# Performance work log

Hardware: AMD Instinct MI355X
Metric: run time of the kernel (lower is better)

## Reference

```python
import jax, jax.numpy as jnp
import numpy as np

N = 100000      # nodes
E = 1600000     # edges (avg degree 16)
F_IN = 128
HID = 128
LAT = 64


def gat_conv(x, src, dst, W, a_src, a_dst, b, n):
    """PyG GATConv (single aggregation): lin -> per-edge LeakyReLU(0.2) attention
    -> segment softmax over incoming edges of each dst node -> weighted scatter-add -> bias.
    W: [F_in, H*C], a_src/a_dst: [H, C], b: [H*C] (concat) or [C] (H=1 either way)."""
    H, C = a_src.shape
    h = (x @ W).reshape(n, H, C)                              # [N,H,C]
    al_s = jnp.einsum('nhc,hc->nh', h, a_src)                 # [N,H]
    al_d = jnp.einsum('nhc,hc->nh', h, a_dst)                 # [N,H]
    e = jax.nn.leaky_relu(al_s[src] + al_d[dst], 0.2)         # [E,H]
    emax = jax.lax.stop_gradient(jax.ops.segment_max(e, dst, num_segments=n))
    ee = jnp.exp(e - emax[dst])                               # stable segment softmax
    den = jax.ops.segment_sum(ee, dst, num_segments=n)
    alpha = ee / (den[dst] + 1e-16)                           # [E,H]
    out = jax.ops.segment_sum(h[src] * alpha[:, :, None], dst, num_segments=n)  # [N,H,C]
    return out.reshape(n, H * C) + b


def setup_inputs() -> dict:
    key = jax.random.key(0)
    ks = jax.random.split(key, 24)
    s = 0.05
    inp = {
        'x': jax.random.normal(ks[0], (N, F_IN), jnp.float32),
        'edge_index': jax.random.randint(ks[1], (2, E), 0, N, jnp.int64),
        # layer 0 GATConv (in -> hid, H=1) + self linear
        'W0': jax.random.normal(ks[2], (F_IN, HID), jnp.float32) * s,
        'a_src0': jax.random.normal(ks[3], (1, HID), jnp.float32) * s,
        'a_dst0': jax.random.normal(ks[4], (1, HID), jnp.float32) * s,
        'b0': jnp.zeros((HID,), jnp.float32),
        'slW0': jax.random.normal(ks[5], (F_IN, HID), jnp.float32) * s,
        'slb0': jnp.zeros((HID,), jnp.float32),
        # layer 1 GATConv (hid -> hid, H=1) + self linear
        'W1': jax.random.normal(ks[6], (HID, HID), jnp.float32) * s,
        'a_src1': jax.random.normal(ks[7], (1, HID), jnp.float32) * s,
        'a_dst1': jax.random.normal(ks[8], (1, HID), jnp.float32) * s,
        'b1': jnp.zeros((HID,), jnp.float32),
        'slW1': jax.random.normal(ks[9], (HID, HID), jnp.float32) * s,
        'slb1': jnp.zeros((HID,), jnp.float32),
        # mu / logvar heads (hid -> lat, H=1, concat=False)
        'Wmu': jax.random.normal(ks[10], (HID, LAT), jnp.float32) * s,
        'a_src_mu': jax.random.normal(ks[11], (1, LAT), jnp.float32) * s,
        'a_dst_mu': jax.random.normal(ks[12], (1, LAT), jnp.float32) * s,
        'b_mu': jnp.zeros((LAT,), jnp.float32),
        'Wlv': jax.random.normal(ks[13], (HID, LAT), jnp.float32) * s,
        'a_src_lv': jax.random.normal(ks[14], (1, LAT), jnp.float32) * s,
        'a_dst_lv': jax.random.normal(ks[15], (1, LAT), jnp.float32) * s,
        'b_lv': jnp.zeros((LAT,), jnp.float32),
    }
    return inp


def reference(x, edge_index, W0, a_src0, a_dst0, b0, slW0, slb0,
              W1, a_src1, a_dst1, b1, slW1, slb1,
              Wmu, a_src_mu, a_dst_mu, b_mu, Wlv, a_src_lv, a_dst_lv, b_lv):
    src, dst = edge_index[0], edge_index[1]
    loop = jnp.arange(N, dtype=edge_index.dtype)
    src_sl = jnp.concatenate([src, loop])   # layers with add_self_loops=True
    dst_sl = jnp.concatenate([dst, loop])
    # layer 0: GATConv(add_self_loops=False) + Linear, then LeakyReLU(0.01)
    h = gat_conv(x, src, dst, W0, a_src0, a_dst0, b0, N) + x @ slW0 + slb0
    h = jax.nn.leaky_relu(h, 0.01)
    # layer 1: GATConv(default self loops) + Linear, then LeakyReLU(0.01)
    h = gat_conv(h, src_sl, dst_sl, W1, a_src1, a_dst1, b1, N) + h @ slW1 + slb1
    h = jax.nn.leaky_relu(h, 0.01)
    mu = gat_conv(h, src_sl, dst_sl, Wmu, a_src_mu, a_dst_mu, b_mu, N)
    logvar = gat_conv(h, src_sl, dst_sl, Wlv, a_src_lv, a_dst_lv, b_lv, N)
    return (mu, logvar)
```

## Files before the change

### kernel.cpp

```cpp
#include <hip/hip_runtime.h>
#include <cstdint>
#include <cstddef>

__device__ __forceinline__ float bf2f(unsigned short u) {
  return __uint_as_float(((unsigned)u) << 16);
}
__device__ __forceinline__ unsigned short f2bf(float f) {
  unsigned u = __float_as_uint(f);
  u = (u + 0x7FFFu + ((u >> 16) & 1u)) >> 16;
  return (unsigned short)u;
}

typedef __attribute__((ext_vector_type(8))) short bf16x8;
typedef __attribute__((ext_vector_type(4))) float f32x4;

__global__ void detect_kernel(const int* __restrict__ ei, int* __restrict__ flag) {
  int any = 0;
  for (int j = threadIdx.x; j < 4096; j += 256) any |= (ei[2 * j + 1] != 0);
  if (any) atomicOr(flag, 1);
}

__device__ __forceinline__ int edge_src(const int* ei, int f, int e, int i) {
  return f ? ei[i] : ei[2 * (size_t)i];
}
__device__ __forceinline__ int edge_dst(const int* ei, int f, int e, int i) {
  return f ? ei[(size_t)e + i] : ei[2 * (size_t)e + 2 * (size_t)i];
}

__global__ void hist_kernel(const int* __restrict__ ei, const int* __restrict__ flag,
                            int* __restrict__ cnt, int e) {
  int i = blockIdx.x * blockDim.x + threadIdx.x;
  if (i < e) atomicAdd(&cnt[edge_dst(ei, *flag, e, i)], 1);
}

__global__ void scan_block(const int* __restrict__ cnt, int* __restrict__ rp,
                           int* __restrict__ bsum, int n) {
  __shared__ int lds[256];
  const int t = threadIdx.x;
  const int base = blockIdx.x * 1024 + t * 4;
  int v0 = (base     < n) ? cnt[base]     : 0;
  int v1 = (base + 1 < n) ? cnt[base + 1] : 0;
  int v2 = (base + 2 < n) ? cnt[base + 2] : 0;
  int v3 = (base + 3 < n) ? cnt[base + 3] : 0;
  int s = v0 + v1 + v2 + v3;
  lds[t] = s;
  __syncthreads();
  for (int off = 1; off < 256; off <<= 1) {
    int y = (t >= off) ? lds[t - off] : 0;
    __syncthreads();
    lds[t] += y;
    __syncthreads();
  }
  int excl = lds[t] - s;
  if (base     < n) rp[base]     = excl;
  if (base + 1 < n) rp[base + 1] = excl + v0;
  if (base + 2 < n) rp[base + 2] = excl + v0 + v1;
  if (base + 3 < n) rp[base + 3] = excl + v0 + v1 + v2;
  if (t == 255) bsum[blockIdx.x] = lds[255];
}

__global__ void scan_tops(int* __restrict__ bsum, int* __restrict__ rp, int nb, int n) {
  __shared__ int lds[128];
  const int t = threadIdx.x;
  int v = (t < nb) ? bsum[t] : 0;
  lds[t] = v;
  __syncthreads();
  for (int off = 1; off < 128; off <<= 1) {
    int y = (t >= off) ? lds[t - off] : 0;
    __syncthreads();
    lds[t] += y;
    __syncthreads();
  }
  if (t < nb) bsum[t] = lds[t] - v;
  if (t == 127) rp[n] = lds[127];
}

__global__ void scan_add(int* __restrict__ rp, const int* __restrict__ bsum, int n) {
  const int base = blockIdx.x * 1024 + threadIdx.x * 4;
  const int add = bsum[blockIdx.x];
#pragma unroll
  for (int i = 0; i < 4; ++i)
    if (base + i < n) rp[base + i] += add;
}

#define NB 128

__global__ void bucket_hist(const int* __restrict__ ei, const int* __restrict__ flag,
                            int* __restrict__ bhist, int e, int W) {
  __shared__ int lh[NB];
  const int t = threadIdx.x;
  if (t < NB) lh[t] = 0;
  __syncthreads();
  const int base = blockIdx.x * 4096;
  const int f = *flag;
  for (int j = t; j < 4096; j += 256) {
    int i = base + j;
    if (i < e) atomicAdd(&lh[edge_dst(ei, f, e, i) / W], 1);
  }
  __syncthreads();
  if (t < NB && lh[t]) atomicAdd(&bhist[t], lh[t]);
}

__global__ void bucket_scan(const int* __restrict__ bhist, int* __restrict__ boffs,
                            int* __restrict__ bcur) {
  __shared__ int lds[NB];
  const int t = threadIdx.x;
  int v = bhist[t];
  lds[t] = v;
  __syncthreads();
  for (int off = 1; off < NB; off <<= 1) {
    int y = (t >= off) ? lds[t - off] : 0;
    __syncthreads();
    lds[t] += y;
    __syncthreads();
  }
  int excl = lds[t] - v;
  boffs[t] = excl;
  bcur[t] = excl;
  if (t == NB - 1) boffs[NB] = lds[NB - 1];
}

__global__ void bucket_scatter(const int* __restrict__ ei, const int* __restrict__ flag,
                               int* __restrict__ bcur, int2* __restrict__ ebuf,
                               int e, int W) {
  __shared__ int lh[NB];
  __shared__ int lbase[NB];
  const int t = threadIdx.x;
  if (t < NB) lh[t] = 0;
  __syncthreads();
  const int base = blockIdx.x * 4096;
  const int f = *flag;
  for (int j = t; j < 4096; j += 256) {
    int i = base + j;
    if (i < e) atomicAdd(&lh[edge_dst(ei, f, e, i) / W], 1);
  }
  __syncthreads();
  if (t < NB) {
    lbase[t] = lh[t] ? atomicAdd(&bcur[t], lh[t]) : 0;
    lh[t] = 0;
  }
  __syncthreads();
  for (int j = t; j < 4096; j += 256) {
    int i = base + j;
    if (i < e) {
      int d = edge_dst(ei, f, e, i);
      int s = edge_src(ei, f, e, i);
      int b = d / W;
      int off = atomicAdd(&lh[b], 1);
      ebuf[lbase[b] + off] = make_int2(s, d);
    }
  }
}

__global__ void bucket_fill(const int2* __restrict__ ebuf, const int* __restrict__ boffs,
                            const int* __restrict__ rp, int* __restrict__ col,
                            int n, int W) {
  __shared__ int cur[1024];
  const int b = blockIdx.x;
  const int lo = b * W;
  const int nn = min(W, n - lo);
  if (nn <= 0) return;
  for (int i = threadIdx.x; i < nn; i += 256) cur[i] = rp[lo + i];
  __syncthreads();
  const int beg = boffs[b], end = boffs[b + 1];
  for (int p = beg + threadIdx.x; p < end; p += 256) {
    int2 sd = ebuf[p];
    int pos = atomicAdd(&cur[sd.y - lo], 1);
    col[pos] = sd.x;
  }
}

__global__ void pack_mfma_b(const float* __restrict__ Wf, unsigned short* __restrict__ Wpk) {
  int i = blockIdx.x * 256 + threadIdx.x;
  if (i >= 2048) return;
  int lane = i & 63, nt = (i >> 6) & 7, ks = i >> 9;
  int nn = lane & 15, q = lane >> 4;
  int k0 = ks * 32 + q * 8, col = nt * 16 + nn;
  unsigned short o[8];
#pragma unroll
  for (int j = 0; j < 8; ++j) o[j] = f2bf(Wf[(size_t)(k0 + j) * 128 + col]);
  uint4 u;
  u.x = (unsigned)o[0] | ((unsigned)o[1] << 16);
  u.y = (unsigned)o[2] | ((unsigned)o[3] << 16);
  u.z = (unsigned)o[4] | ((unsigned)o[5] << 16);
  u.w = (unsigned)o[6] | ((unsigned)o[7] << 16);
  *(uint4*)(Wpk + (size_t)i * 8) = u;
}

__global__ void pack_mfma_head(const float* __restrict__ Wmu, const float* __restrict__ Wlv,
                               unsigned short* __restrict__ Wpk) {
  int i = blockIdx.x * 256 + threadIdx.x;
  if (i >= 2048) return;
  int lane = i & 63, nt = (i >> 6) & 7, ks = i >> 9;
  int nn = lane & 15, q = lane >> 4;
  int k0 = ks * 32 + q * 8, col = nt * 16 + nn;
  unsigned short o[8];
#pragma unroll
  for (int j = 0; j < 8; ++j) {
    float v = (col < 64) ? Wmu[(size_t)(k0 + j) * 64 + col]
                         : Wlv[(size_t)(k0 + j) * 64 + (col - 64)];
    o[j] = f2bf(v);
  }
  uint4 u;
  u.x = (unsigned)o[0] | ((unsigned)o[1] << 16);
  u.y = (unsigned)o[2] | ((unsigned)o[3] << 16);
  u.z = (unsigned)o[4] | ((unsigned)o[5] << 16);
  u.w = (unsigned)o[6] | ((unsigned)o[7] << 16);
  *(uint4*)(Wpk + (size_t)i * 8) = u;
}

template <bool HEAD>
__launch_bounds__(256)
__global__ void gemm_mfma(const float* __restrict__ X, const unsigned short* __restrict__ Wpk,
                          const float* __restrict__ a0s, const float* __restrict__ a0d,
                          const float* __restrict__ a1s, const float* __restrict__ a1d,
                          unsigned short* __restrict__ hg,
                          float* __restrict__ als, float* __restrict__ ald, int n) {
  const int wave = threadIdx.x >> 6;
  const int lane = threadIdx.x & 63;
  const int nidx = lane & 15, q = lane >> 4;
  const int r0 = blockIdx.x * 64 + wave * 16;
  const int arow = r0 + nidx;

  f32x4 acc[8];
#pragma unroll
  for (int nt = 0; nt < 8; ++nt) acc[nt] = (f32x4){0.f, 0.f, 0.f, 0.f};

#pragma unroll
  for (int ks = 0; ks < 4; ++ks) {
    union { unsigned short u[8]; bf16x8 v; } af;
    if (arow < n) {
      const float* xp = X + (size_t)arow * 128 + ks * 32 + q * 8;
      float4 a = *(const float4*)xp;
      float4 b = *(const float4*)(xp + 4);
      af.u[0] = f2bf(a.x); af.u[1] = f2bf(a.y); af.u[2] = f2bf(a.z); af.u[3] = f2bf(a.w);
      af.u[4] = f2bf(b.x); af.u[5] = f2bf(b.y); af.u[6] = f2bf(b.z); af.u[7] = f2bf(b.w);
    } else {
#pragma unroll
      for (int j = 0; j < 8; ++j) af.u[j] = 0;
    }
    const unsigned short* bp = Wpk + ((size_t)ks * 8 * 64 + lane) * 8;
#pragma unroll
    for (int nt = 0; nt < 8; ++nt) {
      bf16x8 bfm = *(const bf16x8*)(bp + (size_t)nt * 64 * 8);
      acc[nt] = __builtin_amdgcn_mfma_f32_16x16x32_bf16(af.v, bfm, acc[nt], 0, 0, 0);
    }
  }

  float dv[8][4];
#pragma unroll
  for (int nt = 0; nt < 8; ++nt) {
#pragma unroll
    for (int r = 0; r < 4; ++r) {
      unsigned short rb = f2bf(acc[nt][r]);
      dv[nt][r] = bf2f(rb);
      int row = r0 + q * 4 + r;
      if (row < n) hg[(size_t)row * 128 + nt * 16 + nidx] = rb;
    }
  }

  if constexpr (!HEAD) {
    float ps[4] = {0, 0, 0, 0}, pd[4] = {0, 0, 0, 0};
#pragma unroll
    for (int nt = 0; nt < 8; ++nt) {
      float as_ = a0s[nt * 16 + nidx];
      float ad_ = a0d[nt * 16 + nidx];
#pragma unroll
      for (int r = 0; r < 4; ++r) {
        ps[r] = fmaf(dv[nt][r], as_, ps[r]);
        pd[r] = fmaf(dv[nt][r], ad_, pd[r]);
      }
    }
#pragma unroll
    for (int r = 0; r < 4; ++r) {
#pragma unroll
      for (int o = 8; o > 0; o >>= 1) {
        ps[r] += __shfl_xor(ps[r], o, 64);
        pd[r] += __shfl_xor(pd[r], o, 64);
      }
      int row = r0 + q * 4 + r;
      if (nidx == 0 && row < n) { als[row] = ps[r]; ald[row] = pd[r]; }
    }
  } else {
    float pms[4] = {0, 0, 0, 0}, pmd[4] = {0, 0, 0, 0};
    float pls[4] = {0, 0, 0, 0}, pld[4] = {0, 0, 0, 0};
#pragma unroll
    for (int nt = 0; nt < 4; ++nt) {
      float as_ = a0s[nt * 16 + nidx];
      float ad_ = a0d[nt * 16 + nidx];
#pragma unroll
      for (int r = 0; r < 4; ++r) {
        pms[r] = fmaf(dv[nt][r], as_, pms[r]);
        pmd[r] = fmaf(dv[nt][r], ad_, pmd[r]);
      }
    }
#pragma unroll
    for (int nt = 4; nt < 8; ++nt) {
      float as_ = a1s[(nt - 4) * 16 + nidx];
      float ad_ = a1d[(nt - 4) * 16 + nidx];
#pragma unroll
      for (int r = 0; r < 4; ++r) {
        pls[r] = fmaf(dv[nt][r], as_, pls[r]);
        pld[r] = fmaf(dv[nt][r], ad_, pld[r]);
      }
    }
#pragma unroll
    for (int r = 0; r < 4; ++r) {
#pragma unroll
      for (int o = 8; o > 0; o >>= 1) {
        pms[r] += __shfl_xor(pms[r], o, 64);
        pmd[r] += __shfl_xor(pmd[r], o, 64);
        pls[r] += __shfl_xor(pls[r], o, 64);
        pld[r] += __shfl_xor(pld[r], o, 64);
      }
      int row = r0 + q * 4 + r;
      if (nidx == 0 && row < n) {
        ((float2*)als)[row] = make_float2(pms[r], pls[r]);
        ((float2*)ald)[row] = make_float2(pmd[r], pld[r]);
      }
    }
  }
}

template <int C, bool YBF>
__launch_bounds__(256)
__global__ void gemm_k128(const float* Xv, const float* __restrict__ Wf,
                          const float* __restrict__ biasf, void* Yv, int n) {
  constexpr int TC = C / 32;
  __shared__ float xs[64 * 32];
  __shared__ float wsm[32 * C];
  const int t = threadIdx.x;
  const int tc = t & 31;
  const int trg = t >> 5;
  const int row0 = blockIdx.x * 64;

  float acc[8][TC];
#pragma unroll
  for (int i = 0; i < 8; ++i)
#pragma unroll
    for (int c = 0; c < TC; ++c) acc[i][c] = 0.f;

  for (int kc = 0; kc < 128; kc += 32) {
    {
      const int r = t >> 2;
      const int j = (t & 3) * 8;
      const int row = row0 + r;
      float v[8];
      if (row < n) {
        const float* xp = Xv + (size_t)row * 128 + kc + j;
        float4 a = *(const float4*)xp;
        float4 b = *(const float4*)(xp + 4);
        v[0] = a.x; v[1] = a.y; v[2] = a.z; v[3] = a.w;
        v[4] = b.x; v[5] = b.y; v[6] = b.z; v[7] = b.w;
      } else {
#pragma unroll
        for (int q = 0; q < 8; ++q) v[q] = 0.f;
      }
      *(float4*)&xs[r * 32 + j]     = make_float4(v[0], v[1], v[2], v[3]);
      *(float4*)&xs[r * 32 + j + 4] = make_float4(v[4], v[5], v[6], v[7]);
    }
    {
      constexpr int per = (32 * C) / 256;
      const float* wp = Wf + (size_t)kc * C + t * per;
      float* wl = wsm + t * per;
#pragma unroll
      for (int q = 0; q < per; q += 4) *(float4*)(wl + q) = *(const float4*)(wp + q);
    }
    __syncthreads();
#pragma unroll
    for (int k = 0; k < 32; k += 4) {
      float wv[4][TC];
#pragma unroll
      for (int k2 = 0; k2 < 4; ++k2) {
        if constexpr (TC == 4) {
          float4 w4 = *(const float4*)&wsm[(k + k2) * C + tc * 4];
          wv[k2][0] = w4.x; wv[k2][1] = w4.y; wv[k2][2] = w4.z; wv[k2][3] = w4.w;
        } else {
          float2 w2 = *(const float2*)&wsm[(k + k2) * C + tc * 2];
          wv[k2][0] = w2.x; wv[k2][1] = w2.y;
        }
      }
#pragma unroll
      for (int i = 0; i < 8; ++i) {
        float4 x4 = *(const float4*)&xs[(trg * 8 + i) * 32 + k];
        float xa[4] = {x4.x, x4.y, x4.z, x4.w};
#pragma unroll
        for (int k2 = 0; k2 < 4; ++k2)
#pragma unroll
          for (int c = 0; c < TC; ++c)
            acc[i][c] = fmaf(xa[k2], wv[k2][c], acc[i][c]);
      }
    }
    __syncthreads();
  }
  float bv[TC];
#pragma unroll
  for (int c = 0; c < TC; ++c) bv[c] = biasf ? biasf[tc * TC + c] : 0.f;
#pragma unroll
  for (int i = 0; i < 8; ++i) {
    const int row = row0 + trg * 8 + i;
    if (row < n) {
      float r[TC];
#pragma unroll
      for (int c = 0; c < TC; ++c) r[c] = acc[i][c] + bv[c];
      if constexpr (YBF) {
        unsigned short* yp = (unsigned short*)Yv + (size_t)row * C + tc * TC;
        if constexpr (TC == 4) {
          uint2 u;
          u.x = (unsigned)f2bf(r[0]) | ((unsigned)f2bf(r[1]) << 16);
          u.y = (unsigned)f2bf(r[2]) | ((unsigned)f2bf(r[3]) << 16);
          *(uint2*)yp = u;
        } else {
          *(unsigned*)yp = (unsigned)f2bf(r[0]) | ((unsigned)f2bf(r[1]) << 16);
        }
      } else {
        float* yp = (float*)Yv + (size_t)row * C + tc * TC;
        if constexpr (TC == 4) *(float4*)yp = make_float4(r[0], r[1], r[2], r[3]);
        else                   *(float2*)yp = make_float2(r[0], r[1]);
      }
    }
  }
}

__launch_bounds__(256)
__global__ void gat_agg3(const unsigned short* __restrict__ hg,
                         const float* __restrict__ als, const float* __restrict__ aldv,
                         const int* __restrict__ rp, const int* __restrict__ col,
                         const float* __restrict__ biasf, float* __restrict__ outv,
                         const float* base, int n, int self_loop, int act) {
  const int node = blockIdx.x * 16 + (threadIdx.x >> 4);
  if (node >= n) return;
  const int g = threadIdx.x & 15;
  const int beg = rp[node];
  const int deg = rp[node + 1] - beg;
  const int total = deg + self_loop;
  const float ad = aldv[node];

  float den = 0.f;
  float acc[8];
#pragma unroll
  for (int k = 0; k < 8; ++k) acc[k] = 0.f;

  const unsigned short* hgl = hg + g * 8;

  for (int cb = 0; cb < total; cb += 16) {
    const int idx = cb + g;
    const bool valid = idx < total;
    int s = node;
    if (valid && idx < deg) s = col[beg + idx];
    float e = 0.f;
    if (valid) {
      float v = als[s] + ad;
      float l = (v > 0.f) ? v : 0.2f * v;
      e = __expf(l);
    }

    const int cnt = (total - cb < 16) ? (total - cb) : 16;
    int j = 0;
    for (; j + 4 <= cnt; j += 4) {
      float w[4]; int ss[4]; uint4 rr[4];
#pragma unroll
      for (int u = 0; u < 4; ++u) { w[u] = __shfl(e, j + u, 16); ss[u] = __shfl(s, j + u, 16); }
#pragma unroll
      for (int u = 0; u < 4; ++u) rr[u] = *(const uint4*)(hgl + (size_t)ss[u] * 128);
#pragma unroll
      for (int u = 0; u < 4; ++u) {
        den += w[u];
        acc[0] = fmaf(w[u], __uint_as_float(rr[u].x << 16),        acc[0]);
        acc[1] = fmaf(w[u], __uint_as_float(rr[u].x & 0xFFFF0000u), acc[1]);
        acc[2] = fmaf(w[u], __uint_as_float(rr[u].y << 16),        acc[2]);
        acc[3] = fmaf(w[u], __uint_as_float(rr[u].y & 0xFFFF0000u), acc[3]);
        acc[4] = fmaf(w[u], __uint_as_float(rr[u].z << 16),        acc[4]);
        acc[5] = fmaf(w[u], __uint_as_float(rr[u].z & 0xFFFF0000u), acc[5]);
        acc[6] = fmaf(w[u], __uint_as_float(rr[u].w << 16),        acc[6]);
        acc[7] = fmaf(w[u], __uint_as_float(rr[u].w & 0xFFFF0000u), acc[7]);
      }
    }
    for (; j < cnt; ++j) {
      float wj = __shfl(e, j, 16);
      int sj = __shfl(s, j, 16);
      uint4 raw = *(const uint4*)(hgl + (size_t)sj * 128);
      den += wj;
      acc[0] = fmaf(wj, __uint_as_float(raw.x << 16),        acc[0]);
      acc[1] = fmaf(wj, __uint_as_float(raw.x & 0xFFFF0000u), acc[1]);
      acc[2] = fmaf(wj, __uint_as_float(raw.y << 16),        acc[2]);
      acc[3] = fmaf(wj, __uint_as_float(raw.y & 0xFFFF0000u), acc[3]);
      acc[4] = fmaf(wj, __uint_as_float(raw.z << 16),        acc[4]);
      acc[5] = fmaf(wj, __uint_as_float(raw.z & 0xFFFF0000u), acc[5]);
      acc[6] = fmaf(wj, __uint_as_float(raw.w << 16),        acc[6]);
      acc[7] = fmaf(wj, __uint_as_float(raw.w & 0xFFFF0000u), acc[7]);
    }
  }

  const float inv = 1.f / (den + 1e-16f);
  const size_t o = (size_t)node * 128 + g * 8;
  float4 bv0 = *(const float4*)(biasf + g * 8);
  float4 bv1 = *(const float4*)(biasf + g * 8 + 4);
  float r[8];
  r[0] = acc[0] * inv + bv0.x; r[1] = acc[1] * inv + bv0.y;
  r[2] = acc[2] * inv + bv0.z; r[3] = acc[3] * inv + bv0.w;
  r[4] = acc[4] * inv + bv1.x; r[5] = acc[5] * inv + bv1.y;
  r[6] = acc[6] * inv + bv1.z; r[7] = acc[7] * inv + bv1.w;
  if (base) {
    float4 s0 = *(const float4*)(base + o);
    float4 s1 = *(const float4*)(base + o + 4);
    r[0] += s0.x; r[1] += s0.y; r[2] += s0.z; r[3] += s0.w;
    r[4] += s1.x; r[5] += s1.y; r[6] += s1.z; r[7] += s1.w;
  }
  if (act) {
#pragma unroll
    for (int k = 0; k < 8; ++k) r[k] = (r[k] > 0.f) ? r[k] : 0.01f * r[k];
  }
  *(float4*)(outv + o)     = make_float4(r[0], r[1], r[2], r[3]);
  *(float4*)(outv + o + 4) = make_float4(r[4], r[5], r[6], r[7]);
}

__launch_bounds__(256)
__global__ void gat_agg_dual(const unsigned short* __restrict__ hg,
                             const float2* __restrict__ alsH, const float2* __restrict__ aldH,
                             const int* __restrict__ rp, const int* __restrict__ col,
                             const float* __restrict__ bmu, const float* __restrict__ blv,
                             float* __restrict__ outF, int n) {
  const int node = blockIdx.x * 16 + (threadIdx.x >> 4);
  if (node >= n) return;
  const int g = threadIdx.x & 15;
  const bool isMu = g < 8;
  const int beg = rp[node];
  const int deg = rp[node + 1] - beg;
  const int total = deg + 1;
  const float2 ad = aldH[node];

  float den = 0.f;
  float acc[8];
#pragma unroll
  for (int k = 0; k < 8; ++k) acc[k] = 0.f;

  const unsigned short* hgl = hg + g * 8;

  for (int cb = 0; cb < total; cb += 16) {
    const int idx = cb + g;
    const bool valid = idx < total;
    int s = node;
    if (valid && idx < deg) s = col[beg + idx];
    float eM = 0.f, eL = 0.f;
    if (valid) {
      float2 as_ = alsH[s];
      float vm = as_.x + ad.x;
      float vl = as_.y + ad.y;
      eM = __expf((vm > 0.f) ? vm : 0.2f * vm);
      eL = __expf((vl > 0.f) ? vl : 0.2f * vl);
    }

    const int cnt = (total - cb < 16) ? (total - cb) : 16;
    int j = 0;
    for (; j + 4 <= cnt; j += 4) {
      float w[4]; int ss[4]; uint4 rr[4];
#pragma unroll
      for (int u = 0; u < 4; ++u) {
        float wm = __shfl(eM, j + u, 16), wl = __shfl(eL, j + u, 16);
        w[u] = isMu ? wm : wl;
        ss[u] = __shfl(s, j + u, 16);
      }
#pragma unroll
      for (int u = 0; u < 4; ++u) rr[u] = *(const uint4*)(hgl + (size_t)ss[u] * 128);
#pragma unroll
      for (int u = 0; u < 4; ++u) {
        den += w[u];
        acc[0] = fmaf(w[u], __uint_as_float(rr[u].x << 16),        acc[0]);
        acc[1] = fmaf(w[u], __uint_as_float(rr[u].x & 0xFFFF0000u), acc[1]);
        acc[2] = fmaf(w[u], __uint_as_float(rr[u].y << 16),        acc[2]);
        acc[3] = fmaf(w[u], __uint_as_float(rr[u].y & 0xFFFF0000u), acc[3]);
        acc[4] = fmaf(w[u], __uint_as_float(rr[u].z << 16),        acc[4]);
        acc[5] = fmaf(w[u], __uint_as_float(rr[u].z & 0xFFFF0000u), acc[5]);
        acc[6] = fmaf(w[u], __uint_as_float(rr[u].w << 16),        acc[6]);
        acc[7] = fmaf(w[u], __uint_as_float(rr[u].w & 0xFFFF0000u), acc[7]);
      }
    }
    for (; j < cnt; ++j) {
      float wm = __shfl(eM, j, 16), wl = __shfl(eL, j, 16);
      float wj = isMu ? wm : wl;
      int sj = __shfl(s, j, 16);
      uint4 raw = *(const uint4*)(hgl + (size_t)sj * 128);
      den += wj;
      acc[0] = fmaf(wj, __uint_as_float(raw.x << 16),        acc[0]);
      acc[1] = fmaf(wj, __uint_as_float(raw.x & 0xFFFF0000u), acc[1]);
      acc[2] = fmaf(wj, __uint_as_float(raw.y << 16),        acc[2]);
      acc[3] = fmaf(wj, __uint_as_float(raw.y & 0xFFFF0000u), acc[3]);
      acc[4] = fmaf(wj, __uint_as_float(raw.z << 16),        acc[4]);
      acc[5] = fmaf(wj, __uint_as_float(raw.z & 0xFFFF0000u), acc[5]);
      acc[6] = fmaf(wj, __uint_as_float(raw.w << 16),        acc[6]);
      acc[7] = fmaf(wj, __uint_as_float(raw.w & 0xFFFF0000u), acc[7]);
    }
  }

  const float inv = 1.f / (den + 1e-16f);
  const int c = (g & 7) * 8;
  const float* bb = isMu ? bmu : blv;
  float4 bv0 = *(const float4*)(bb + c);
  float4 bv1 = *(const float4*)(bb + c + 4);
  float* op = outF + (isMu ? (size_t)0 : (size_t)n * 64) + (size_t)node * 64 + c;
  *(float4*)op = make_float4(acc[0] * inv + bv0.x, acc[1] * inv + bv0.y,
                             acc[2] * inv + bv0.z, acc[3] * inv + bv0.w);
  *(float4*)(op + 4) = make_float4(acc[4] * inv + bv1.x, acc[5] * inv + bv1.y,
                                   acc[6] * inv + bv1.z, acc[7] * inv + bv1.w);
}

extern "C" void kernel_launch(void* const* d_in, const int* in_sizes, int n_in,
                              void* d_out, int out_size, void* d_ws, size_t ws_size,
                              hipStream_t stream) {
  const int N = in_sizes[0] / 128;
  const int E = in_sizes[1] / 2;
  const int W = (N + NB - 1) / NB;

  const float* x    = (const float*)d_in[0];
  const int*   ei   = (const int*)d_in[1];
  const float* W0   = (const float*)d_in[2];
  const float* as0  = (const float*)d_in[3];
  const float* ad0  = (const float*)d_in[4];
  const float* b0   = (const float*)d_in[5];
  const float* slW0 = (const float*)d_in[6];
  const float* slb0 = (const float*)d_in[7];
  const float* W1   = (const float*)d_in[8];
  const float* as1  = (const float*)d_in[9];
  const float* ad1  = (const float*)d_in[10];
  const float* b1   = (const float*)d_in[11];
  const float* slW1 = (const float*)d_in[12];
  const float* slb1 = (const float*)d_in[13];
  const float* Wmu  = (const float*)d_in[14];
  const float* asmu = (const float*)d_in[15];
  const float* admu = (const float*)d_in[16];
  const float* bmu  = (const float*)d_in[17];
  const float* Wlv  = (const float*)d_in[18];
  const float* aslv = (const float*)d_in[19];
  const float* adlv = (const float*)d_in[20];
  const float* blv  = (const float*)d_in[21];

  float*          outF = (float*)d_out;
  unsigned short* hgB  = (unsigned short*)d_out;

  char* w = (char*)d_ws;
  auto carve = [&](size_t bytes) -> char* {
    char* p = w;
    w += (bytes + 255) & ~(size_t)255;
    return p;
  };
  float*          h0    = (float*)carve((size_t)N * 128 * 4);
  unsigned short* hgHd  = (unsigned short*)carve((size_t)N * 128 * 2);
  float*          als   = (float*)carve((size_t)N * 4);
  float*          ald   = (float*)carve((size_t)N * 4);
  float2*         alsH  = (float2*)carve((size_t)N * 8);
  float2*         aldH  = (float2*)carve((size_t)N * 8);
  int*            cnt   = (int*)carve((size_t)N * 4);
  int*            rp    = (int*)carve((size_t)(N + 1) * 4);
  int*            col   = (int*)carve((size_t)E * 4);
  int*            bsum  = (int*)carve(512);
  int*            bhist = (int*)carve(NB * 4);
  int*            boffs = (int*)carve((NB + 1) * 4);
  int*            bcur  = (int*)carve(NB * 4);
  int*            flag  = (int*)carve(4);
  unsigned short* Wpk0  = (unsigned short*)carve(2048 * 8 * 2);
  unsigned short* Wpk1  = (unsigned short*)carve(2048 * 8 * 2);
  unsigned short* Wpkh  = (unsigned short*)carve(2048 * 8 * 2);
  int2*           ebuf  = (int2*)h0;

  const int gE  = (E + 255) / 256;
  const int gB4 = (E + 4095) / 4096;
  const int gG  = (N + 63) / 64;
  const int gW  = (N + 15) / 16;
  const int nb  = (N + 1023) / 1024;

  hipMemsetAsync(flag, 0, 4, stream);
  hipMemsetAsync(cnt, 0, (size_t)N * 4, stream);
  hipMemsetAsync(bhist, 0, NB * 4, stream);
  detect_kernel<<<1, 256, 0, stream>>>(ei, flag);
  hist_kernel<<<gE, 256, 0, stream>>>(ei, flag, cnt, E);
  bucket_hist<<<gB4, 256, 0, stream>>>(ei, flag, bhist, E, W);
  scan_block<<<nb, 256, 0, stream>>>(cnt, rp, bsum, N);
  scan_tops<<<1, 128, 0, stream>>>(bsum, rp, nb, N);
  scan_add<<<nb, 256, 0, stream>>>(rp, bsum, N);
  bucket_scan<<<1, NB, 0, stream>>>(bhist, boffs, bcur);
  bucket_scatter<<<gB4, 256, 0, stream>>>(ei, flag, bcur, ebuf, E, W);
  bucket_fill<<<NB, 256, 0, stream>>>(ebuf, boffs, rp, col, N, W);

  pack_mfma_b<<<8, 256, 0, stream>>>(W0, Wpk0);
  pack_mfma_b<<<8, 256, 0, stream>>>(W1, Wpk1);
  pack_mfma_head<<<8, 256, 0, stream>>>(Wmu, Wlv, Wpkh);

  gemm_mfma<false><<<gG, 256, 0, stream>>>(x, Wpk0, as0, ad0, nullptr, nullptr,
                                           hgB, als, ald, N);
  gemm_k128<128, false><<<gG, 256, 0, stream>>>(x, slW0, slb0, h0, N);
  gat_agg3<<<gW, 256, 0, stream>>>(hgB, als, ald, rp, col, b0, h0, h0, N, 0, 1);

  gemm_mfma<false><<<gG, 256, 0, stream>>>(h0, Wpk1, as1, ad1, nullptr, nullptr,
                                           hgB, als, ald, N);
  gemm_k128<128, false><<<gG, 256, 0, stream>>>(h0, slW1, slb1, h0, N);
  gat_agg3<<<gW, 256, 0, stream>>>(hgB, als, ald, rp, col, b1, h0, h0, N, 1, 1);

  gemm_mfma<true><<<gG, 256, 0, stream>>>(h0, Wpkh, asmu, admu, aslv, adlv,
                                          hgHd, (float*)alsH, (float*)aldH, N);
  gat_agg_dual<<<gW, 256, 0, stream>>>(hgHd, alsH, aldH, rp, col, bmu, blv, outF, N);
}
```

Before: 671.3 us.

## Precompute per-edge attention weights in separate kernels and prefetch next edge chunk

Adds edge_w and edge_w_dual kernels that compute exp(leaky_relu(als[src]+ald[dst])) for each CSR edge into a buffer that aliases existing workspace. The aggregation kernels then read these weights coalesced instead of doing a dependent gather of als[col] followed by exp. They also software-prefetch the next 16-edge chunk's column indices and weights while the current chunk is processed, to hide the latency of the dependent load chain. The cost is extra kernel launches plus an extra write and read of an E-sized weight array per layer, and the one-thread-per-node edge_w loop is itself uncoalesced and load-imbalanced.

After: 720.4 us. +7.3%, slower.

```diff
diff --git a/kernel.cpp b/kernel.cpp
--- a/kernel.cpp
+++ b/kernel.cpp
@@ -167,6 +167,34 @@
     int2 sd = ebuf[p];
     int pos = atomicAdd(&cur[sd.y - lo], 1);
     col[pos] = sd.x;
+  }
+}
+
+__global__ void edge_w(const float* __restrict__ als, const float* __restrict__ ald,
+                       const int* __restrict__ rp, const int* __restrict__ col,
+                       float* __restrict__ ew, int n) {
+  int i = blockIdx.x * 256 + threadIdx.x;
+  if (i >= n) return;
+  const int b = rp[i], e = rp[i + 1];
+  const float ad = ald[i];
+  for (int p = b; p < e; ++p) {
+    float v = als[col[p]] + ad;
+    ew[p] = __expf((v > 0.f) ? v : 0.2f * v);
+  }
+}
+
+__global__ void edge_w_dual(const float2* __restrict__ alsH, const float2* __restrict__ aldH,
+                            const int* __restrict__ rp, const int* __restrict__ col,
+                            float2* __restrict__ ewH, int n) {
+  int i = blockIdx.x * 256 + threadIdx.x;
+  if (i >= n) return;
+  const int b = rp[i], e = rp[i + 1];
+  const float2 ad = aldH[i];
+  for (int p = b; p < e; ++p) {
+    float2 a = alsH[col[p]];
+    float vm = a.x + ad.x, vl = a.y + ad.y;
+    ewH[p] = make_float2(__expf((vm > 0.f) ? vm : 0.2f * vm),
+                         __expf((vl > 0.f) ? vl : 0.2f * vl));
   }
 }
 
@@ -424,6 +452,7 @@
 
 __launch_bounds__(256)
 __global__ void gat_agg3(const unsigned short* __restrict__ hg,
+                         const float* __restrict__ ew,
                          const float* __restrict__ als, const float* __restrict__ aldv,
                          const int* __restrict__ rp, const int* __restrict__ col,
                          const float* __restrict__ biasf, float* __restrict__ outv,
@@ -434,7 +463,12 @@
   const int beg = rp[node];
   const int deg = rp[node + 1] - beg;
   const int total = deg + self_loop;
-  const float ad = aldv[node];
+
+  float wself = 0.f;
+  if (self_loop) {
+    float v = als[node] + aldv[node];
+    wself = __expf((v > 0.f) ? v : 0.2f * v);
+  }
 
   float den = 0.f;
   float acc[8];
@@ -443,16 +477,19 @@
 
   const unsigned short* hgl = hg + g * 8;
 
+  int sA = node; float wA = 0.f;
+  {
+    const int idx = g;
+    if (idx < deg)        { sA = col[beg + idx]; wA = ew[beg + idx]; }
+    else if (idx < total) { wA = wself; }
+  }
+
   for (int cb = 0; cb < total; cb += 16) {
-    const int idx = cb + g;
-    const bool valid = idx < total;
-    int s = node;
-    if (valid && idx < deg) s = col[beg + idx];
-    float e = 0.f;
-    if (valid) {
-      float v = als[s] + ad;
-      float l = (v > 0.f) ? v : 0.2f * v;
-      e = __expf(l);
+    int sB = node; float wB = 0.f;
+    {
+      const int idx = cb + 16 + g;
+      if (idx < deg)        { sB = col[beg + idx]; wB = ew[beg + idx]; }
+      else if (idx < total) { wB = wself; }
     }
 
     const int cnt = (total - cb < 16) ? (total - cb) : 16;
@@ -460,7 +497,7 @@
     for (; j + 4 <= cnt; j += 4) {
       float w[4]; int ss[4]; uint4 rr[4];
 #pragma unroll
-      for (int u = 0; u < 4; ++u) { w[u] = __shfl(e, j + u, 16); ss[u] = __shfl(s, j + u, 16); }
+      for (int u = 0; u < 4; ++u) { w[u] = __shfl(wA, j + u, 16); ss[u] = __shfl(sA, j + u, 16); }
 #pragma unroll
       for (int u = 0; u < 4; ++u) rr[u] = *(const uint4*)(hgl + (size_t)ss[u] * 128);
 #pragma unroll
@@ -477,8 +514,8 @@
       }
     }
     for (; j < cnt; ++j) {
-      float wj = __shfl(e, j, 16);
-      int sj = __shfl(s, j, 16);
+      float wj = __shfl(wA, j, 16);
+      int sj = __shfl(sA, j, 16);
       uint4 raw = *(const uint4*)(hgl + (size_t)sj * 128);
       den += wj;
       acc[0] = fmaf(wj, __uint_as_float(raw.x << 16),        acc[0]);
@@ -490,6 +527,7 @@
       acc[6] = fmaf(wj, __uint_as_float(raw.w << 16),        acc[6]);
       acc[7] = fmaf(wj, __uint_as_float(raw.w & 0xFFFF0000u), acc[7]);
     }
+    sA = sB; wA = wB;
   }
 
   const float inv = 1.f / (den + 1e-16f);
@@ -517,6 +555,7 @@
 
 __launch_bounds__(256)
 __global__ void gat_agg_dual(const unsigned short* __restrict__ hg,
+                             const float2* __restrict__ ewH,
                              const float2* __restrict__ alsH, const float2* __restrict__ aldH,
                              const int* __restrict__ rp, const int* __restrict__ col,
                              const float* __restrict__ bmu, const float* __restrict__ blv,
@@ -528,7 +567,14 @@
   const int beg = rp[node];
   const int deg = rp[node + 1] - beg;
   const int total = deg + 1;
-  const float2 ad = aldH[node];
+
+  float wselfM, wselfL;
+  {
+    float2 a_ = alsH[node], d_ = aldH[node];
+    float vm = a_.x + d_.x, vl = a_.y + d_.y;
+    wselfM = __expf((vm > 0.f) ? vm : 0.2f * vm);
+    wselfL = __expf((vl > 0.f) ? vl : 0.2f * vl);
+  }
 
   float den = 0.f;
   float acc[8];
@@ -537,18 +583,19 @@
 
   const unsigned short* hgl = hg + g * 8;
 
+  int sA = node; float eMA = 0.f, eLA = 0.f;
+  {
+    const int idx = g;
+    if (idx < deg)        { sA = col[beg + idx]; float2 e2 = ewH[beg + idx]; eMA = e2.x; eLA = e2.y; }
+    else if (idx < total) { eMA = wselfM; eLA = wselfL; }
+  }
+
   for (int cb = 0; cb < total; cb += 16) {
-    const int idx = cb + g;
-    const bool valid = idx < total;
-    int s = node;
-    if (valid && idx < deg) s = col[beg + idx];
-    float eM = 0.f, eL = 0.f;
-    if (valid) {
-      float2 as_ = alsH[s];
-      float vm = as_.x + ad.x;
-      float vl = as_.y + ad.y;
-      eM = __expf((vm > 0.f) ? vm : 0.2f * vm);
-      eL = __expf((vl > 0.f) ? vl : 0.2f * vl);
+    int sB = node; float eMB = 0.f, eLB = 0.f;
+    {
+      const int idx = cb + 16 + g;
+      if (idx < deg)        { sB = col[beg + idx]; float2 e2 = ewH[beg + idx]; eMB = e2.x; eLB = e2.y; }
+      else if (idx < total) { eMB = wselfM; eLB = wselfL; }
     }
 
     const int cnt = (total - cb < 16) ? (total - cb) : 16;
@@ -557,9 +604,9 @@
       float w[4]; int ss[4]; uint4 rr[4];
 #pragma unroll
       for (int u = 0; u < 4; ++u) {
-        float wm = __shfl(eM, j + u, 16), wl = __shfl(eL, j + u, 16);
+        float wm = __shfl(eMA, j + u, 16), wl = __shfl(eLA, j + u, 16);
         w[u] = isMu ? wm : wl;
-        ss[u] = __shfl(s, j + u, 16);
+        ss[u] = __shfl(sA, j + u, 16);
       }
 #pragma unroll
       for (int u = 0; u < 4; ++u) rr[u] = *(const uint4*)(hgl + (size_t)ss[u] * 128);
@@ -577,9 +624,9 @@
       }
     }
     for (; j < cnt; ++j) {
-      float wm = __shfl(eM, j, 16), wl = __shfl(eL, j, 16);
+      float wm = __shfl(eMA, j, 16), wl = __shfl(eLA, j, 16);
       float wj = isMu ? wm : wl;
-      int sj = __shfl(s, j, 16);
+      int sj = __shfl(sA, j, 16);
       uint4 raw = *(const uint4*)(hgl + (size_t)sj * 128);
       den += wj;
       acc[0] = fmaf(wj, __uint_as_float(raw.x << 16),        acc[0]);
@@ -591,6 +638,7 @@
       acc[6] = fmaf(wj, __uint_as_float(raw.w << 16),        acc[6]);
       acc[7] = fmaf(wj, __uint_as_float(raw.w & 0xFFFF0000u), acc[7]);
     }
+    sA = sB; eMA = eMB; eLA = eLB;
   }
 
   const float inv = 1.f / (den + 1e-16f);
@@ -662,11 +710,14 @@
   unsigned short* Wpk1  = (unsigned short*)carve(2048 * 8 * 2);
   unsigned short* Wpkh  = (unsigned short*)carve(2048 * 8 * 2);
   int2*           ebuf  = (int2*)h0;
+  float*          ew    = (float*)hgHd;
+  float2*         ewH   = (float2*)h0;
 
   const int gE  = (E + 255) / 256;
   const int gB4 = (E + 4095) / 4096;
   const int gG  = (N + 63) / 64;
   const int gW  = (N + 15) / 16;
+  const int gN  = (N + 255) / 256;
   const int nb  = (N + 1023) / 1024;
 
   hipMemsetAsync(flag, 0, 4, stream);
@@ -688,15 +739,18 @@
 
   gemm_mfma<false><<<gG, 256, 0, stream>>>(x, Wpk0, as0, ad0, nullptr, nullptr,
                                            hgB, als, ald, N);
+  edge_w<<<gN, 256, 0, stream>>>(als, ald, rp, col, ew, N);
   gemm_k128<128, false><<<gG, 256, 0, stream>>>(x, slW0, slb0, h0, N);
-  gat_agg3<<<gW, 256, 0, stream>>>(hgB, als, ald, rp, col, b0, h0, h0, N, 0, 1);
+  gat_agg3<<<gW, 256, 0, stream>>>(hgB, ew, als, ald, rp, col, b0, h0, h0, N, 0, 1);
 
   gemm_mfma<false><<<gG, 256, 0, stream>>>(h0, Wpk1, as1, ad1, nullptr, nullptr,
                                            hgB, als, ald, N);
+  edge_w<<<gN, 256, 0, stream>>>(als, ald, rp, col, ew, N);
   gemm_k128<128, false><<<gG, 256, 0, stream>>>(h0, slW1, slb1, h0, N);
-  gat_agg3<<<gW, 256, 0, stream>>>(hgB, als, ald, rp, col, b1, h0, h0, N, 1, 1);
+  gat_agg3<<<gW, 256, 0, stream>>>(hgB, ew, als, ald, rp, col, b1, h0, h0, N, 1, 1);
 
   gemm_mfma<true><<<gG, 256, 0, stream>>>(h0, Wpkh, asmu, admu, aslv, adlv,
                                           hgHd, (float*)alsH, (float*)aldH, N);
-  gat_agg_dual<<<gW, 256, 0, stream>>>(hgHd, alsH, aldH, rp, col, bmu, blv, outF, N);
-}
+  edge_w_dual<<<gN, 256, 0, stream>>>(alsH, aldH, rp, col, ewH, N);
+  gat_agg_dual<<<gW, 256, 0, stream>>>(hgHd, ewH, alsH, aldH, rp, col, bmu, blv, outF, N);
+}
```

## Fuse self-linear GEMM into MFMA GEMM using split-bf16 hi/lo products

Applied to the files above, without the earlier changes.

Replaces the separate fp32 SIMT self-linear GEMM with extra MFMA accumulators inside the attention-projection GEMM kernel. The input row is read once and split into bf16 hi/lo parts, and the self weights are pre-packed as hi/lo pairs. Three MFMAs (hh, lh, hl) approximate fp32 accuracy. This removes one kernel launch and a second pass over X. In exchange it adds register pressure (16 accumulators) and roughly four times the MFMA work per tile.

Result: faster. 648.8 us (-3.4%).

```diff
diff --git a/kernel.cpp b/kernel.cpp
--- a/kernel.cpp
+++ b/kernel.cpp
@@ -187,6 +187,35 @@
   *(uint4*)(Wpk + (size_t)i * 8) = u;
 }
 
+__global__ void pack_mfma_b_hilo(const float* __restrict__ Wf,
+                                 unsigned short* __restrict__ Hi,
+                                 unsigned short* __restrict__ Lo) {
+  int i = blockIdx.x * 256 + threadIdx.x;
+  if (i >= 2048) return;
+  int lane = i & 63, nt = (i >> 6) & 7, ks = i >> 9;
+  int nn = lane & 15, q = lane >> 4;
+  int k0 = ks * 32 + q * 8, col = nt * 16 + nn;
+  unsigned short oh[8], ol[8];
+#pragma unroll
+  for (int j = 0; j < 8; ++j) {
+    float v = Wf[(size_t)(k0 + j) * 128 + col];
+    unsigned short h = f2bf(v);
+    oh[j] = h;
+    ol[j] = f2bf(v - bf2f(h));
+  }
+  uint4 uh, ul;
+  uh.x = (unsigned)oh[0] | ((unsigned)oh[1] << 16);
+  uh.y = (unsigned)oh[2] | ((unsigned)oh[3] << 16);
+  uh.z = (unsigned)oh[4] | ((unsigned)oh[5] << 16);
+  uh.w = (unsigned)oh[6] | ((unsigned)oh[7] << 16);
+  ul.x = (unsigned)ol[0] | ((unsigned)ol[1] << 16);
+  ul.y = (unsigned)ol[2] | ((unsigned)ol[3] << 16);
+  ul.z = (unsigned)ol[4] | ((unsigned)ol[5] << 16);
+  ul.w = (unsigned)ol[6] | ((unsigned)ol[7] << 16);
+  *(uint4*)(Hi + (size_t)i * 8) = uh;
+  *(uint4*)(Lo + (size_t)i * 8) = ul;
+}
+
 __global__ void pack_mfma_head(const float* __restrict__ Wmu, const float* __restrict__ Wlv,
                                unsigned short* __restrict__ Wpk) {
   int i = blockIdx.x * 256 + threadIdx.x;
@@ -209,13 +238,111 @@
   *(uint4*)(Wpk + (size_t)i * 8) = u;
 }
 
-template <bool HEAD>
 __launch_bounds__(256)
-__global__ void gemm_mfma(const float* __restrict__ X, const unsigned short* __restrict__ Wpk,
-                          const float* __restrict__ a0s, const float* __restrict__ a0d,
-                          const float* __restrict__ a1s, const float* __restrict__ a1d,
-                          unsigned short* __restrict__ hg,
-                          float* __restrict__ als, float* __restrict__ ald, int n) {
+__global__ void gemm_fused(const float* __restrict__ X, const unsigned short* __restrict__ Wpk,
+                           const unsigned short* __restrict__ Sph, const unsigned short* __restrict__ Spl,
+                           const float* __restrict__ a0s, const float* __restrict__ a0d,
+                           const float* __restrict__ slb,
+                           unsigned short* __restrict__ hg, float* __restrict__ hself,
+                           float* __restrict__ als, float* __restrict__ ald, int n) {
+  const int wave = threadIdx.x >> 6;
+  const int lane = threadIdx.x & 63;
+  const int nidx = lane & 15, q = lane >> 4;
+  const int r0 = blockIdx.x * 64 + wave * 16;
+  const int arow = r0 + nidx;
+
+  f32x4 acc[8], accS[8];
+#pragma unroll
+  for (int nt = 0; nt < 8; ++nt) {
+    acc[nt]  = (f32x4){0.f, 0.f, 0.f, 0.f};
+    accS[nt] = (f32x4){0.f, 0.f, 0.f, 0.f};
+  }
+
+#pragma unroll
+  for (int ks = 0; ks < 4; ++ks) {
+    union { unsigned short u[8]; bf16x8 v; } afh, afl;
+    if (arow < n) {
+      const float* xp = X + (size_t)arow * 128 + ks * 32 + q * 8;
+      float4 a = *(const float4*)xp;
+      float4 b = *(const float4*)(xp + 4);
+      float xv[8] = {a.x, a.y, a.z, a.w, b.x, b.y, b.z, b.w};
+#pragma unroll
+      for (int j = 0; j < 8; ++j) {
+        unsigned short h = f2bf(xv[j]);
+        afh.u[j] = h;
+        afl.u[j] = f2bf(xv[j] - bf2f(h));
+      }
+    } else {
+#pragma unroll
+      for (int j = 0; j < 8; ++j) { afh.u[j] = 0; afl.u[j] = 0; }
+    }
+    const size_t base = ((size_t)ks * 8 * 64 + lane) * 8;
+    const unsigned short* bp = Wpk + base;
+    const unsigned short* ph = Sph + base;
+    const unsigned short* pl = Spl + base;
+#pragma unroll
+    for (int nt = 0; nt < 8; ++nt) {
+      bf16x8 bW = *(const bf16x8*)(bp + (size_t)nt * 64 * 8);
+      acc[nt] = __builtin_amdgcn_mfma_f32_16x16x32_bf16(afh.v, bW, acc[nt], 0, 0, 0);
+      bf16x8 bH = *(const bf16x8*)(ph + (size_t)nt * 64 * 8);
+      bf16x8 bL = *(const bf16x8*)(pl + (size_t)nt * 64 * 8);
+      accS[nt] = __builtin_amdgcn_mfma_f32_16x16x32_bf16(afh.v, bH, accS[nt], 0, 0, 0);
+      accS[nt] = __builtin_amdgcn_mfma_f32_16x16x32_bf16(afl.v, bH, accS[nt], 0, 0, 0);
+      accS[nt] = __builtin_amdgcn_mfma_f32_16x16x32_bf16(afh.v, bL, accS[nt], 0, 0, 0);
+    }
+  }
+
+  float dv[8][4];
+#pragma unroll
+  for (int nt = 0; nt < 8; ++nt) {
+#pragma unroll
+    for (int r = 0; r < 4; ++r) {
+      unsigned short rb = f2bf(acc[nt][r]);
+      dv[nt][r] = bf2f(rb);
+      int row = r0 + q * 4 + r;
+      if (row < n) hg[(size_t)row * 128 + nt * 16 + nidx] = rb;
+    }
+  }
+
+#pragma unroll
+  for (int nt = 0; nt < 8; ++nt) {
+    const float sb = slb[nt * 16 + nidx];
+#pragma unroll
+    for (int r = 0; r < 4; ++r) {
+      int row = r0 + q * 4 + r;
+      if (row < n) hself[(size_t)row * 128 + nt * 16 + nidx] = accS[nt][r] + sb;
+    }
+  }
+
+  float ps[4] = {0, 0, 0, 0}, pd[4] = {0, 0, 0, 0};
+#pragma unroll
+  for (int nt = 0; nt < 8; ++nt) {
+    float as_ = a0s[nt * 16 + nidx];
+    float ad_ = a0d[nt * 16 + nidx];
+#pragma unroll
+    for (int r = 0; r < 4; ++r) {
+      ps[r] = fmaf(dv[nt][r], as_, ps[r]);
+      pd[r] = fmaf(dv[nt][r], ad_, pd[r]);
+    }
+  }
+#pragma unroll
+  for (int r = 0; r < 4; ++r) {
+#pragma unroll
+    for (int o = 8; o > 0; o >>= 1) {
+      ps[r] += __shfl_xor(ps[r], o, 64);
+      pd[r] += __shfl_xor(pd[r], o, 64);
+    }
+    int row = r0 + q * 4 + r;
+    if (nidx == 0 && row < n) { als[row] = ps[r]; ald[row] = pd[r]; }
+  }
+}
+
+__launch_bounds__(256)
+__global__ void gemm_mfma_head(const float* __restrict__ X, const unsigned short* __restrict__ Wpk,
+                               const float* __restrict__ a0s, const float* __restrict__ a0d,
+                               const float* __restrict__ a1s, const float* __restrict__ a1d,
+                               unsigned short* __restrict__ hg,
+                               float* __restrict__ als, float* __restrict__ ald, int n) {
   const int wave = threadIdx.x >> 6;
   const int lane = threadIdx.x & 63;
   const int nidx = lane & 15, q = lane >> 4;
@@ -259,165 +386,41 @@
     }
   }
 
-  if constexpr (!HEAD) {
-    float ps[4] = {0, 0, 0, 0}, pd[4] = {0, 0, 0, 0};
-#pragma unroll
-    for (int nt = 0; nt < 8; ++nt) {
-      float as_ = a0s[nt * 16 + nidx];
-      float ad_ = a0d[nt * 16 + nidx];
-#pragma unroll
-      for (int r = 0; r < 4; ++r) {
-        ps[r] = fmaf(dv[nt][r], as_, ps[r]);
-        pd[r] = fmaf(dv[nt][r], ad_, pd[r]);
-      }
-    }
+  float pms[4] = {0, 0, 0, 0}, pmd[4] = {0, 0, 0, 0};
+  float pls[4] = {0, 0, 0, 0}, pld[4] = {0, 0, 0, 0};
+#pragma unroll
+  for (int nt = 0; nt < 4; ++nt) {
+    float as_ = a0s[nt * 16 + nidx];
+    float ad_ = a0d[nt * 16 + nidx];
 #pragma unroll
     for (int r = 0; r < 4; ++r) {
-#pragma unroll
-      for (int o = 8; o > 0; o >>= 1) {
-        ps[r] += __shfl_xor(ps[r], o, 64);
-        pd[r] += __shfl_xor(pd[r], o, 64);
-      }
-      int row = r0 + q * 4 + r;
-      if (nidx == 0 && row < n) { als[row] = ps[r]; ald[row] = pd[r]; }
-    }
-  } else {
-    float pms[4] = {0, 0, 0, 0}, pmd[4] = {0, 0, 0, 0};
-    float pls[4] = {0, 0, 0, 0}, pld[4] = {0, 0, 0, 0};
-#pragma unroll
-    for (int nt = 0; nt < 4; ++nt) {
-      float as_ = a0s[nt * 16 + nidx];
-      float ad_ = a0d[nt * 16 + nidx];
-#pragma unroll
-      for (int r = 0; r < 4; ++r) {
-        pms[r] = fmaf(dv[nt][r], as_, pms[r]);
-        pmd[r] = fmaf(dv[nt][r], ad_, pmd[r]);
-      }
-    }
-#pragma unroll
-    for (int nt = 4; nt < 8; ++nt) {
-      float as_ = a1s[(nt - 4) * 16 + nidx];
-      float ad_ = a1d[(nt - 4) * 16 + nidx];
-#pragma unroll
-      for (int r = 0; r < 4; ++r) {
-        pls[r] = fmaf(dv[nt][r], as_, pls[r]);
-        pld[r] = fmaf(dv[nt][r], ad_, pld[r]);
-      }
-    }
+      pms[r] = fmaf(dv[nt][r], as_, pms[r]);
+      pmd[r] = fmaf(dv[nt][r], ad_, pmd[r]);
+    }
+  }
+#pragma unroll
+  for (int nt = 4; nt < 8; ++nt) {
+    float as_ = a1s[(nt - 4) * 16 + nidx];
+    float ad_ = a1d[(nt - 4) * 16 + nidx];
 #pragma unroll
     for (int r = 0; r < 4; ++r) {
-#pragma unroll
-      for (int o = 8; o > 0; o >>= 1) {
-        pms[r] += __shfl_xor(pms[r], o, 64);
-        pmd[r] += __shfl_xor(pmd[r], o, 64);
-        pls[r] += __shfl_xor(pls[r], o, 64);
-        pld[r] += __shfl_xor(pld[r], o, 64);
-      }
-      int row = r0 + q * 4 + r;
-      if (nidx == 0 && row < n) {
-        ((float2*)als)[row] = make_float2(pms[r], pls[r]);
-        ((float2*)ald)[row] = make_float2(pmd[r], pld[r]);
-      }
-    }
-  }
-}
-
-template <int C, bool YBF>
-__launch_bounds__(256)
-__global__ void gemm_k128(const float* Xv, const float* __restrict__ Wf,
-                          const float* __restrict__ biasf, void* Yv, int n) {
-  constexpr int TC = C / 32;
-  __shared__ float xs[64 * 32];
-  __shared__ float wsm[32 * C];
-  const int t = threadIdx.x;
-  const int tc = t & 31;
-  const int trg = t >> 5;
-  const int row0 = blockIdx.x * 64;
-
-  float acc[8][TC];
-#pragma unroll
-  for (int i = 0; i < 8; ++i)
-#pragma unroll
-    for (int c = 0; c < TC; ++c) acc[i][c] = 0.f;
-
-  for (int kc = 0; kc < 128; kc += 32) {
-    {
-      const int r = t >> 2;
-      const int j = (t & 3) * 8;
-      const int row = row0 + r;
-      float v[8];
-      if (row < n) {
-        const float* xp = Xv + (size_t)row * 128 + kc + j;
-        float4 a = *(const float4*)xp;
-        float4 b = *(const float4*)(xp + 4);
-        v[0] = a.x; v[1] = a.y; v[2] = a.z; v[3] = a.w;
-        v[4] = b.x; v[5] = b.y; v[6] = b.z; v[7] = b.w;
-      } else {
-#pragma unroll
-        for (int q = 0; q < 8; ++q) v[q] = 0.f;
-      }
-      *(float4*)&xs[r * 32 + j]     = make_float4(v[0], v[1], v[2], v[3]);
-      *(float4*)&xs[r * 32 + j + 4] = make_float4(v[4], v[5], v[6], v[7]);
-    }
-    {
-      constexpr int per = (32 * C) / 256;
-      const float* wp = Wf + (size_t)kc * C + t * per;
-      float* wl = wsm + t * per;
-#pragma unroll
-      for (int q = 0; q < per; q += 4) *(float4*)(wl + q) = *(const float4*)(wp + q);
-    }
-    __syncthreads();
-#pragma unroll
-    for (int k = 0; k < 32; k += 4) {
-      float wv[4][TC];
-#pragma unroll
-      for (int k2 = 0; k2 < 4; ++k2) {
-        if constexpr (TC == 4) {
-          float4 w4 = *(const float4*)&wsm[(k + k2) * C + tc * 4];
-          wv[k2][0] = w4.x; wv[k2][1] = w4.y; wv[k2][2] = w4.z; wv[k2][3] = w4.w;
-        } else {
-          float2 w2 = *(const float2*)&wsm[(k + k2) * C + tc * 2];
-          wv[k2][0] = w2.x; wv[k2][1] = w2.y;
-        }
-      }
-#pragma unroll
-      for (int i = 0; i < 8; ++i) {
-        float4 x4 = *(const float4*)&xs[(trg * 8 + i) * 32 + k];
-        float xa[4] = {x4.x, x4.y, x4.z, x4.w};
-#pragma unroll
-        for (int k2 = 0; k2 < 4; ++k2)
-#pragma unroll
-          for (int c = 0; c < TC; ++c)
-            acc[i][c] = fmaf(xa[k2], wv[k2][c], acc[i][c]);
-      }
-    }
-    __syncthreads();
-  }
-  float bv[TC];
-#pragma unroll
-  for (int c = 0; c < TC; ++c) bv[c] = biasf ? biasf[tc * TC + c] : 0.f;
-#pragma unroll
-  for (int i = 0; i < 8; ++i) {
-    const int row = row0 + trg * 8 + i;
-    if (row < n) {
-      float r[TC];
-#pragma unroll
-      for (int c = 0; c < TC; ++c) r[c] = acc[i][c] + bv[c];
-      if constexpr (YBF) {
-        unsigned short* yp = (unsigned short*)Yv + (size_t)row * C + tc * TC;
-        if constexpr (TC == 4) {
-          uint2 u;
-          u.x = (unsigned)f2bf(r[0]) | ((unsigned)f2bf(r[1]) << 16);
-          u.y = (unsigned)f2bf(r[2]) | ((unsigned)f2bf(r[3]) << 16);
-          *(uint2*)yp = u;
-        } else {
-          *(unsigned*)yp = (unsigned)f2bf(r[0]) | ((unsigned)f2bf(r[1]) << 16);
-        }
-      } else {
-        float* yp = (float*)Yv + (size_t)row * C + tc * TC;
-        if constexpr (TC == 4) *(float4*)yp = make_float4(r[0], r[1], r[2], r[3]);
-        else                   *(float2*)yp = make_float2(r[0], r[1]);
-      }
+      pls[r] = fmaf(dv[nt][r], as_, pls[r]);
+      pld[r] = fmaf(dv[nt][r], ad_, pld[r]);
+    }
+  }
+#pragma unroll
+  for (int r = 0; r < 4; ++r) {
+#pragma unroll
+    for (int o = 8; o > 0; o >>= 1) {
+      pms[r] += __shfl_xor(pms[r], o, 64);
+      pmd[r] += __shfl_xor(pmd[r], o, 64);
+      pls[r] += __shfl_xor(pls[r], o, 64);
+      pld[r] += __shfl_xor(pld[r], o, 64);
+    }
+    int row = r0 + q * 4 + r;
+    if (nidx == 0 && row < n) {
+      ((float2*)als)[row] = make_float2(pms[r], pls[r]);
+      ((float2*)ald)[row] = make_float2(pmd[r], pld[r]);
     }
   }
 }
@@ -661,6 +664,10 @@
   unsigned short* Wpk0  = (unsigned short*)carve(2048 * 8 * 2);
   unsigned short* Wpk1  = (unsigned short*)carve(2048 * 8 * 2);
   unsigned short* Wpkh  = (unsigned short*)carve(2048 * 8 * 2);
+  unsigned short* Spk0h = (unsigned short*)carve(2048 * 8 * 2);
+  unsigned short* Spk0l = (unsigned short*)carve(2048 * 8 * 2);
+  unsigned short* Spk1h = (unsigned short*)carve(2048 * 8 * 2);
+  unsigned short* Spk1l = (unsigned short*)carve(2048 * 8 * 2);
   int2*           ebuf  = (int2*)h0;
 
   const int gE  = (E + 255) / 256;
@@ -684,19 +691,19 @@
 
   pack_mfma_b<<<8, 256, 0, stream>>>(W0, Wpk0);
   pack_mfma_b<<<8, 256, 0, stream>>>(W1, Wpk1);
+  pack_mfma_b_hilo<<<8, 256, 0, stream>>>(slW0, Spk0h, Spk0l);
+  pack_mfma_b_hilo<<<8, 256, 0, stream>>>(slW1, Spk1h, Spk1l);
   pack_mfma_head<<<8, 256, 0, stream>>>(Wmu, Wlv, Wpkh);
 
-  gemm_mfma<false><<<gG, 256, 0, stream>>>(x, Wpk0, as0, ad0, nullptr, nullptr,
-                                           hgB, als, ald, N);
-  gemm_k128<128, false><<<gG, 256, 0, stream>>>(x, slW0, slb0, h0, N);
+  gemm_fused<<<gG, 256, 0, stream>>>(x, Wpk0, Spk0h, Spk0l, as0, ad0, slb0,
+                                     hgB, h0, als, ald, N);
   gat_agg3<<<gW, 256, 0, stream>>>(hgB, als, ald, rp, col, b0, h0, h0, N, 0, 1);
 
-  gemm_mfma<false><<<gG, 256, 0, stream>>>(h0, Wpk1, as1, ad1, nullptr, nullptr,
-                                           hgB, als, ald, N);
-  gemm_k128<128, false><<<gG, 256, 0, stream>>>(h0, slW1, slb1, h0, N);
+  gemm_fused<<<gG, 256, 0, stream>>>(h0, Wpk1, Spk1h, Spk1l, as1, ad1, slb1,
+                                     hgB, h0, als, ald, N);
   gat_agg3<<<gW, 256, 0, stream>>>(hgB, als, ald, rp, col, b1, h0, h0, N, 1, 1);
 
-  gemm_mfma<true><<<gG, 256, 0, stream>>>(h0, Wpkh, asmu, admu, aslv, adlv,
-                                          hgHd, (float*)alsH, (float*)aldH, N);
+  gemm_mfma_head<<<gG, 256, 0, stream>>>(h0, Wpkh, asmu, admu, aslv, adlv,
+                                         hgHd, (float*)alsH, (float*)aldH, N);
   gat_agg_dual<<<gW, 256, 0, stream>>>(hgHd, alsH, aldH, rp, col, bmu, blv, outF, N);
 }
```
